# Kernel tuning notes

Hardware: AMD Instinct MI355X
Metric: run time of the kernel (lower is better)

Reference implementation:

```python
import jax, jax.numpy as jnp
import numpy as np

D_IN = 1024
D_OUT = 1024
SEQ = 2048
BATCH = 4


def setup_inputs() -> dict:
    key = jax.random.key(0)
    k_x, k_q, k_k, k_v = jax.random.split(key, 4)
    scale = 1.0 / np.sqrt(D_IN)  # ~ torch Linear init scale
    x = jax.random.normal(k_x, (BATCH, SEQ, D_IN), dtype=jnp.float32)
    # torch nn.Linear weights have shape [d_out, d_in]; y = x @ W.T
    Wq = jax.random.uniform(k_q, (D_OUT, D_IN), jnp.float32, -scale, scale)
    Wk = jax.random.uniform(k_k, (D_OUT, D_IN), jnp.float32, -scale, scale)
    Wv = jax.random.uniform(k_v, (D_OUT, D_IN), jnp.float32, -scale, scale)
    return {"x": x, "Wq": Wq, "Wk": Wk, "Wv": Wv}


def reference(x, Wq, Wk, Wv):
    # projections (no bias, qkv_bias=False)
    q = jnp.einsum("bsd,ed->bse", x, Wq)  # [B,S,D_OUT]
    k = jnp.einsum("bsd,ed->bse", x, Wk)
    v = jnp.einsum("bsd,ed->bse", x, Wv)
    scores = jnp.einsum("bqe,bke->bqk", q, k)  # [B,S,S]
    seq = scores.shape[-1]
    causal = jnp.tril(jnp.ones((seq, seq), dtype=bool))  # keep lower-tri
    scores = jnp.where(causal[None], scores, -jnp.inf)
    # note: original scales AFTER masking: softmax(scores / sqrt(d_k))
    inv_sqrt_dk = 1.0 / np.sqrt(k.shape[-1]).astype(np.float32)
    weights = jax.nn.softmax(scores * inv_sqrt_dk, axis=-1)
    # dropout p=0.0 (eval-equivalent): identity
    return jnp.einsum("bqk,bke->bqe", weights, v)
```

## Files before the change

### kernel.cpp

```cpp
#include <hip/hip_runtime.h>
#include <hip/hip_bf16.h>

typedef __bf16 v8bf __attribute__((ext_vector_type(8)));
typedef float v4f __attribute__((ext_vector_type(4)));

#define GBL_AS(p) ((const __attribute__((address_space(1))) unsigned int*)(p))
#define LDS_AS(p) ((__attribute__((address_space(3))) unsigned int*)(p))

__global__ void cast_f32_bf16(const float* __restrict__ src,
                              __hip_bfloat16* __restrict__ dst, int n) {
  int i = (blockIdx.x * 256 + threadIdx.x) * 4;
  if (i >= n) return;
  float4 f = *(const float4*)(src + i);
  union { __hip_bfloat16 h[4]; uint2 u; } pk;
  pk.h[0] = __float2bfloat16(f.x);
  pk.h[1] = __float2bfloat16(f.y);
  pk.h[2] = __float2bfloat16(f.z);
  pk.h[3] = __float2bfloat16(f.w);
  *(uint2*)(dst + i) = pk.u;
}

__global__ void transpose_bf16(const __hip_bfloat16* __restrict__ src,
                               __hip_bfloat16* __restrict__ dst,
                               int rows, int cols) {
  __shared__ __hip_bfloat16 t[32][33];
  long boff = (long)blockIdx.z * rows * cols;
  src += boff; dst += boff;
  int c0 = blockIdx.x * 32, r0 = blockIdx.y * 32;
  int x = threadIdx.x;
#pragma unroll
  for (int i = 0; i < 4; ++i) {
    int y = threadIdx.y + i * 8;
    t[y][x] = src[(long)(r0 + y) * cols + (c0 + x)];
  }
  __syncthreads();
#pragma unroll
  for (int i = 0; i < 4; ++i) {
    int y = threadIdx.y + i * 8;
    dst[(long)(c0 + y) * rows + (r0 + x)] = t[x][y];
  }
}

template<bool OUT_BF16>
__global__ __launch_bounds__(256, 2)
void gemm_nt(const __hip_bfloat16* __restrict__ A, long sAb, int lda,
             const __hip_bfloat16* __restrict__ B, long sBb, int ldb,
             void* __restrict__ Cv, long sCb, int ldc,
             int K, float scale, int causal_mode) {
  const int tid = threadIdx.x;
  const int l = tid & 63, w = tid >> 6;
  const int nb = blockIdx.x * 128, mb = blockIdx.y * 128;
  if (causal_mode == 1 && nb > mb + 127) return;
  int kend = K;
  if (causal_mode == 2) kend = (K < mb + 128) ? K : (mb + 128);

  A += (long)blockIdx.z * sAb;
  B += (long)blockIdx.z * sBb;

  __shared__ alignas(16) __hip_bfloat16 As[128 * 32];
  __shared__ alignas(16) __hip_bfloat16 Bs[128 * 32];

  v4f acc[4][4] = {};
  const int wm = (w >> 1) * 64, wn = (w & 1) * 64;

  for (int k0 = 0; k0 < kend; k0 += 32) {
#pragma unroll
    for (int t = 0; t < 2; ++t) {
      const int cbase = t * 256 + w * 64;
      const int c = cbase + l;
      const int row = c >> 2, col = (c & 3) << 3;
      __builtin_amdgcn_global_load_lds(
          GBL_AS(A + (long)(mb + row) * lda + (k0 + col)),
          LDS_AS(As + cbase * 8), 16, 0, 0);
      __builtin_amdgcn_global_load_lds(
          GBL_AS(B + (long)(nb + row) * ldb + (k0 + col)),
          LDS_AS(Bs + cbase * 8), 16, 0, 0);
    }
    __syncthreads();

    v8bf af[4], bfr[4];
#pragma unroll
    for (int i = 0; i < 4; ++i) {
      af[i]  = *(const v8bf*)(As + (wm + i * 16 + (l & 15)) * 32 + ((l >> 4) << 3));
      bfr[i] = *(const v8bf*)(Bs + (wn + i * 16 + (l & 15)) * 32 + ((l >> 4) << 3));
    }
#pragma unroll
    for (int i = 0; i < 4; ++i)
#pragma unroll
      for (int j = 0; j < 4; ++j)
        acc[i][j] = __builtin_amdgcn_mfma_f32_16x16x32_bf16(af[i], bfr[j], acc[i][j], 0, 0, 0);
    __syncthreads();
  }

  const int col0 = nb + wn + (l & 15);
  const int row0 = mb + wm + ((l >> 4) << 2);
  if constexpr (OUT_BF16) {
    __hip_bfloat16* C = (__hip_bfloat16*)Cv + (long)blockIdx.z * sCb;
#pragma unroll
    for (int i = 0; i < 4; ++i)
#pragma unroll
      for (int r = 0; r < 4; ++r) {
        long ro = (long)(row0 + i * 16 + r) * ldc;
#pragma unroll
        for (int j = 0; j < 4; ++j)
          C[ro + col0 + j * 16] = __float2bfloat16(acc[i][j][r] * scale);
      }
  } else {
    float* C = (float*)Cv + (long)blockIdx.z * sCb;
#pragma unroll
    for (int i = 0; i < 4; ++i)
#pragma unroll
      for (int r = 0; r < 4; ++r) {
        long ro = (long)(row0 + i * 16 + r) * ldc;
#pragma unroll
        for (int j = 0; j < 4; ++j)
          C[ro + col0 + j * 16] = acc[i][j][r] * scale;
      }
  }
}

__global__ __launch_bounds__(256)
void softmax_causal(float* __restrict__ scores) {
  const int row = blockIdx.x;
  const int q = row & 2047;
  float* s = scores + (long)row * 2048;
  __hip_bfloat16* wout = (__hip_bfloat16*)s;
  const int tid = threadIdx.x, l = tid & 63, w = tid >> 6;

  float v[8];
#pragma unroll
  for (int i = 0; i < 8; ++i) {
    int c = tid + i * 256;
    v[i] = (c <= q) ? s[c] : -__builtin_inff();
  }
  float m = v[0];
#pragma unroll
  for (int i = 1; i < 8; ++i) m = fmaxf(m, v[i]);
#pragma unroll
  for (int off = 32; off > 0; off >>= 1) m = fmaxf(m, __shfl_down(m, off));
  __shared__ float redm[4], reds[4];
  if (l == 0) redm[w] = m;
  __syncthreads();
  m = fmaxf(fmaxf(redm[0], redm[1]), fmaxf(redm[2], redm[3]));

  float e[8];
  float sum = 0.f;
#pragma unroll
  for (int i = 0; i < 8; ++i) { e[i] = expf(v[i] - m); sum += e[i]; }
#pragma unroll
  for (int off = 32; off > 0; off >>= 1) sum += __shfl_down(sum, off);
  if (l == 0) reds[w] = sum;
  __syncthreads();
  sum = reds[0] + reds[1] + reds[2] + reds[3];
  float inv = 1.0f / sum;
#pragma unroll
  for (int i = 0; i < 8; ++i) {
    int c = tid + i * 256;
    wout[c] = __float2bfloat16(e[i] * inv);
  }
}

extern "C" void kernel_launch(void* const* d_in, const int* in_sizes, int n_in,
                              void* d_out, int out_size, void* d_ws, size_t ws_size,
                              hipStream_t stream) {
  const float* x  = (const float*)d_in[0];
  const float* Wq = (const float*)d_in[1];
  const float* Wk = (const float*)d_in[2];
  const float* Wv = (const float*)d_in[3];
  float* out = (float*)d_out;
  char* ws = (char*)d_ws;

  __hip_bfloat16* qkv = (__hip_bfloat16*)ws;
  __hip_bfloat16* vT  = (__hip_bfloat16*)(ws + 50331648);
  __hip_bfloat16* xb  = (__hip_bfloat16*)(ws + 67108864);
  __hip_bfloat16* Wb  = (__hip_bfloat16*)(ws + 83886080);
  float* scores       = (float*)(ws + 67108864);

  cast_f32_bf16<<<8192, 256, 0, stream>>>(x, xb, 8388608);
  cast_f32_bf16<<<1024, 256, 0, stream>>>(Wq, Wb,            1048576);
  cast_f32_bf16<<<1024, 256, 0, stream>>>(Wk, Wb + 1048576,  1048576);
  cast_f32_bf16<<<1024, 256, 0, stream>>>(Wv, Wb + 2097152,  1048576);

  gemm_nt<true><<<dim3(8, 64, 3), 256, 0, stream>>>(
      xb, 0L, 1024, Wb, 1048576L, 1024, qkv, 8388608L, 1024,
      1024, 1.0f, 0);

  transpose_bf16<<<dim3(32, 64, 4), dim3(32, 8), 0, stream>>>(
      qkv + 16777216, vT, 2048, 1024);

  gemm_nt<false><<<dim3(16, 16, 4), 256, 0, stream>>>(
      qkv, 2097152L, 1024, qkv + 8388608, 2097152L, 1024,
      scores, 4194304L, 2048, 1024, 0.03125f, 1);

  softmax_causal<<<8192, 256, 0, stream>>>(scores);

  gemm_nt<false><<<dim3(8, 16, 4), 256, 0, stream>>>(
      (__hip_bfloat16*)scores, 8388608L, 4096, vT, 2097152L, 2048,
      out, 2097152L, 1024, 2048, 1.0f, 2);
}
```

Baseline: 288.4 us.

## Fuse exp into QK^T epilogue, defer softmax normalization to PV GEMM

```diff
diff --git a/kernel.cpp b/kernel.cpp
--- a/kernel.cpp
+++ b/kernel.cpp
@@ -20,6 +20,20 @@
   *(uint2*)(dst + i) = pk.u;
 }
 
+__global__ void cast_w3(const float* __restrict__ a, const float* __restrict__ b,
+                        const float* __restrict__ c, __hip_bfloat16* __restrict__ dst) {
+  int seg = blockIdx.x >> 10;
+  const float* src = seg == 0 ? a : (seg == 1 ? b : c);
+  int i = ((blockIdx.x & 1023) * 256 + threadIdx.x) * 4;
+  float4 f = *(const float4*)(src + i);
+  union { __hip_bfloat16 h[4]; uint2 u; } pk;
+  pk.h[0] = __float2bfloat16(f.x);
+  pk.h[1] = __float2bfloat16(f.y);
+  pk.h[2] = __float2bfloat16(f.z);
+  pk.h[3] = __float2bfloat16(f.w);
+  *(uint2*)(dst + seg * 1048576 + i) = pk.u;
+}
+
 __global__ void transpose_bf16(const __hip_bfloat16* __restrict__ src,
                                __hip_bfloat16* __restrict__ dst,
                                int rows, int cols) {
@@ -41,21 +55,24 @@
   }
 }
 
-template<bool OUT_BF16>
+template<int MODE>
 __global__ __launch_bounds__(256, 2)
 void gemm_nt(const __hip_bfloat16* __restrict__ A, long sAb, int lda,
              const __hip_bfloat16* __restrict__ B, long sBb, int ldb,
              void* __restrict__ Cv, long sCb, int ldc,
-             int K, float scale, int causal_mode) {
+             int K, float scale, const float* __restrict__ inv_sums) {
   const int tid = threadIdx.x;
   const int l = tid & 63, w = tid >> 6;
-  const int nb = blockIdx.x * 128, mb = blockIdx.y * 128;
-  if (causal_mode == 1 && nb > mb + 127) return;
+  int z, nb;
+  if (MODE == 0) { z = blockIdx.x >> 3; nb = (blockIdx.x & 7) << 7; }
+  else           { z = blockIdx.z;      nb = blockIdx.x << 7; }
+  const int mb = blockIdx.y * 128;
+  if (MODE == 1 && nb > mb + 127) return;
   int kend = K;
-  if (causal_mode == 2) kend = (K < mb + 128) ? K : (mb + 128);
-
-  A += (long)blockIdx.z * sAb;
-  B += (long)blockIdx.z * sBb;
+  if (MODE == 2) kend = (K < mb + 128) ? K : (mb + 128);
+
+  A += (long)z * sAb;
+  B += (long)z * sBb;
 
   __shared__ alignas(16) __hip_bfloat16 As[128 * 32];
   __shared__ alignas(16) __hip_bfloat16 Bs[128 * 32];
@@ -94,8 +111,8 @@
 
   const int col0 = nb + wn + (l & 15);
   const int row0 = mb + wm + ((l >> 4) << 2);
-  if constexpr (OUT_BF16) {
-    __hip_bfloat16* C = (__hip_bfloat16*)Cv + (long)blockIdx.z * sCb;
+  if constexpr (MODE == 0) {
+    __hip_bfloat16* C = (__hip_bfloat16*)Cv + (long)z * sCb;
 #pragma unroll
     for (int i = 0; i < 4; ++i)
 #pragma unroll
@@ -105,59 +122,56 @@
         for (int j = 0; j < 4; ++j)
           C[ro + col0 + j * 16] = __float2bfloat16(acc[i][j][r] * scale);
       }
+  } else if constexpr (MODE == 1) {
+    __hip_bfloat16* C = (__hip_bfloat16*)Cv + (long)z * sCb;
+#pragma unroll
+    for (int i = 0; i < 4; ++i)
+#pragma unroll
+      for (int r = 0; r < 4; ++r) {
+        const int m = row0 + i * 16 + r;
+        long ro = (long)m * ldc;
+#pragma unroll
+        for (int j = 0; j < 4; ++j) {
+          const int n = col0 + j * 16;
+          float p = (n <= m) ? __expf(acc[i][j][r] * scale) : 0.0f;
+          C[ro + n] = __float2bfloat16(p);
+        }
+      }
   } else {
-    float* C = (float*)Cv + (long)blockIdx.z * sCb;
+    float* C = (float*)Cv + (long)z * sCb;
+    const float* inv = inv_sums + z * 2048;
 #pragma unroll
     for (int i = 0; i < 4; ++i)
 #pragma unroll
       for (int r = 0; r < 4; ++r) {
-        long ro = (long)(row0 + i * 16 + r) * ldc;
+        const int m = row0 + i * 16 + r;
+        const float s = inv[m];
+        long ro = (long)m * ldc;
 #pragma unroll
         for (int j = 0; j < 4; ++j)
-          C[ro + col0 + j * 16] = acc[i][j][r] * scale;
+          C[ro + col0 + j * 16] = acc[i][j][r] * s;
       }
   }
 }
 
 __global__ __launch_bounds__(256)
-void softmax_causal(float* __restrict__ scores) {
-  const int row = blockIdx.x;
+void rowsum_inv(const __hip_bfloat16* __restrict__ P, float* __restrict__ inv) {
+  const int w = threadIdx.x >> 6, l = threadIdx.x & 63;
+  const int row = blockIdx.x * 4 + w;
   const int q = row & 2047;
-  float* s = scores + (long)row * 2048;
-  __hip_bfloat16* wout = (__hip_bfloat16*)s;
-  const int tid = threadIdx.x, l = tid & 63, w = tid >> 6;
-
-  float v[8];
-#pragma unroll
-  for (int i = 0; i < 8; ++i) {
-    int c = tid + i * 256;
-    v[i] = (c <= q) ? s[c] : -__builtin_inff();
-  }
-  float m = v[0];
-#pragma unroll
-  for (int i = 1; i < 8; ++i) m = fmaxf(m, v[i]);
-#pragma unroll
-  for (int off = 32; off > 0; off >>= 1) m = fmaxf(m, __shfl_down(m, off));
-  __shared__ float redm[4], reds[4];
-  if (l == 0) redm[w] = m;
-  __syncthreads();
-  m = fmaxf(fmaxf(redm[0], redm[1]), fmaxf(redm[2], redm[3]));
-
-  float e[8];
+  const int rend = ((q >> 7) + 1) << 7;
+  const __hip_bfloat16* p = P + (long)row * 2048;
   float sum = 0.f;
-#pragma unroll
-  for (int i = 0; i < 8; ++i) { e[i] = expf(v[i] - m); sum += e[i]; }
+  for (int c0 = l * 8; c0 < rend; c0 += 512) {
+    union { v8bf v; unsigned short us[8]; } u;
+    u.v = *(const v8bf*)(p + c0);
+#pragma unroll
+    for (int j = 0; j < 8; ++j)
+      sum += __uint_as_float((unsigned)u.us[j] << 16);
+  }
 #pragma unroll
   for (int off = 32; off > 0; off >>= 1) sum += __shfl_down(sum, off);
-  if (l == 0) reds[w] = sum;
-  __syncthreads();
-  sum = reds[0] + reds[1] + reds[2] + reds[3];
-  float inv = 1.0f / sum;
-#pragma unroll
-  for (int i = 0; i < 8; ++i) {
-    int c = tid + i * 256;
-    wout[c] = __float2bfloat16(e[i] * inv);
-  }
+  if (l == 0) inv[row] = 1.0f / sum;
 }
 
 extern "C" void kernel_launch(void* const* d_in, const int* in_sizes, int n_in,
@@ -174,27 +188,26 @@
   __hip_bfloat16* vT  = (__hip_bfloat16*)(ws + 50331648);
   __hip_bfloat16* xb  = (__hip_bfloat16*)(ws + 67108864);
   __hip_bfloat16* Wb  = (__hip_bfloat16*)(ws + 83886080);
-  float* scores       = (float*)(ws + 67108864);
+  __hip_bfloat16* P   = (__hip_bfloat16*)(ws + 67108864);
+  float* inv          = (float*)(ws + 100663296);
 
   cast_f32_bf16<<<8192, 256, 0, stream>>>(x, xb, 8388608);
-  cast_f32_bf16<<<1024, 256, 0, stream>>>(Wq, Wb,            1048576);
-  cast_f32_bf16<<<1024, 256, 0, stream>>>(Wk, Wb + 1048576,  1048576);
-  cast_f32_bf16<<<1024, 256, 0, stream>>>(Wv, Wb + 2097152,  1048576);
-
-  gemm_nt<true><<<dim3(8, 64, 3), 256, 0, stream>>>(
+  cast_w3<<<3072, 256, 0, stream>>>(Wq, Wk, Wv, Wb);
+
+  gemm_nt<0><<<dim3(24, 64, 1), 256, 0, stream>>>(
       xb, 0L, 1024, Wb, 1048576L, 1024, qkv, 8388608L, 1024,
-      1024, 1.0f, 0);
+      1024, 1.0f, nullptr);
 
   transpose_bf16<<<dim3(32, 64, 4), dim3(32, 8), 0, stream>>>(
       qkv + 16777216, vT, 2048, 1024);
 
-  gemm_nt<false><<<dim3(16, 16, 4), 256, 0, stream>>>(
+  gemm_nt<1><<<dim3(16, 16, 4), 256, 0, stream>>>(
       qkv, 2097152L, 1024, qkv + 8388608, 2097152L, 1024,
-      scores, 4194304L, 2048, 1024, 0.03125f, 1);
-
-  softmax_causal<<<8192, 256, 0, stream>>>(scores);
-
-  gemm_nt<false><<<dim3(8, 16, 4), 256, 0, stream>>>(
-      (__hip_bfloat16*)scores, 8388608L, 4096, vT, 2097152L, 2048,
-      out, 2097152L, 1024, 2048, 1.0f, 2);
-}
+      P, 4194304L, 2048, 1024, 0.03125f, nullptr);
+
+  rowsum_inv<<<2048, 256, 0, stream>>>(P, inv);
+
+  gemm_nt<2><<<dim3(8, 16, 4), 256, 0, stream>>>(
+      P, 4194304L, 2048, vT, 2097152L, 2048,
+      out, 2097152L, 1024, 2048, 1.0f, inv);
+}
```

After: 263.6 us. 1.09x faster.
